# Kernel optimization log

Measured on AMD Instinct MI355X. Metric: run time of the kernel, lower is better.

## Reference

```python
import jax, jax.numpy as jnp
import numpy as np

DN = ('NCHW', 'OIHW', 'NCHW')

def conv2d(x, w, b, stride, pad):
    y = jax.lax.conv_general_dilated(x, w, (stride, stride), ((pad, pad), (pad, pad)), dimension_numbers=DN)
    return y + b[None, :, None, None]

def convt2d(x, w, b):
    # torch ConvTranspose2d(k=4, stride=2, padding=1); torch weight layout [Cin, Cout, kH, kW]
    wf = jnp.flip(w, (2, 3)).transpose(1, 0, 2, 3)  # -> [Cout, Cin, kH, kW]
    y = jax.lax.conv_general_dilated(x, wf, (1, 1), ((2, 2), (2, 2)), lhs_dilation=(2, 2), dimension_numbers=DN)
    return y + b[None, :, None, None]

def setup_inputs() -> dict:
    key = jax.random.key(0)
    ks = jax.random.split(key, 20)
    Hc, E, K = 128, 256, 8192
    s = lambda k, shape, fan: jax.random.normal(k, shape, jnp.float32) * (1.0 / np.sqrt(fan))
    inp = {
        'x': jax.random.normal(ks[0], (4, 3, 256, 256), jnp.float32),
        'enc_w1': s(ks[1], (Hc, 3, 4, 4), 3 * 16), 'enc_b1': jnp.zeros((Hc,), jnp.float32),
        'enc_w2': s(ks[2], (Hc, Hc, 4, 4), Hc * 16), 'enc_b2': jnp.zeros((Hc,), jnp.float32),
        'enc_w3': s(ks[3], (Hc, Hc, 3, 3), Hc * 9), 'enc_b3': jnp.zeros((Hc,), jnp.float32),
        'qconv_w': s(ks[4], (E, Hc, 1, 1), Hc), 'qconv_b': jnp.zeros((E,), jnp.float32),
        'codebook': jax.random.uniform(ks[5], (K, E), jnp.float32, -1.0 / K, 1.0 / K),
        'pqconv_w': s(ks[6], (Hc, E, 1, 1), E), 'pqconv_b': jnp.zeros((Hc,), jnp.float32),
        'dec_w1': s(ks[7], (Hc, Hc, 3, 3), Hc * 9), 'dec_b1': jnp.zeros((Hc,), jnp.float32),
        'dect_w2': s(ks[8], (Hc, Hc, 4, 4), Hc * 16), 'dect_b2': jnp.zeros((Hc,), jnp.float32),
        'dect_w3': s(ks[9], (Hc, 3, 4, 4), Hc * 16), 'dect_b3': jnp.zeros((3,), jnp.float32),
    }
    return inp

def quantize(z, codebook):
    B, C, H, W = z.shape
    zf = z.transpose(0, 2, 3, 1).reshape(-1, C)  # [N, C]
    d = (jnp.sum(zf * zf, axis=1, keepdims=True)
         + jnp.sum(codebook * codebook, axis=1)
         - 2.0 * zf @ codebook.T)  # [N, K]
    indices = jnp.argmin(d, axis=1)
    quant = codebook[indices].reshape(B, H, W, C).transpose(0, 3, 1, 2)
    commit_loss = jnp.mean((jax.lax.stop_gradient(quant) - z) ** 2)
    quant = z + jax.lax.stop_gradient(quant - z)  # straight-through
    return quant, indices, commit_loss

def reference(x, enc_w1, enc_b1, enc_w2, enc_b2, enc_w3, enc_b3, qconv_w, qconv_b,
              codebook, pqconv_w, pqconv_b, dec_w1, dec_b1, dect_w2, dect_b2, dect_w3, dect_b3):
    h = jax.nn.relu(conv2d(x, enc_w1, enc_b1, 2, 1))
    h = jax.nn.relu(conv2d(h, enc_w2, enc_b2, 2, 1))
    h = conv2d(h, enc_w3, enc_b3, 1, 1)
    h = conv2d(h, qconv_w, qconv_b, 1, 0)
    quant, indices, commit_loss = quantize(h, codebook)
    q = conv2d(quant, pqconv_w, pqconv_b, 1, 0)
    d = jax.nn.relu(conv2d(q, dec_w1, dec_b1, 1, 1))
    d = jax.nn.relu(convt2d(d, dect_w2, dect_b2))
    recon = convt2d(d, dect_w3, dect_b3)
    return recon, commit_loss, indices
```

## Files before the change

### kernel.cpp

```cpp
#include <hip/hip_runtime.h>

#define OFF_A     ((size_t)0)
#define OFF_BINFO ((size_t)8388608)
#define OFF_B     ((size_t)34611200)
#define OFF_C     ((size_t)43532288)
#define OFF_D     ((size_t)52453376)
#define OFF_E     ((size_t)69230592)
#define OFF_ZN    ((size_t)81813504)
#define OFF_CN    ((size_t)81879040)
#define OFF_IDX   ((size_t)81911808)
#define OFF_ACC   ((size_t)81977344)
#define OFF_WR2   ((size_t)81977600)
#define OFF_WR3   ((size_t)83026176)
#define OFF_QWT   ((size_t)83050752)
#define OFF_WD2   ((size_t)83181824)
#define OFF_WD3   ((size_t)85278976)
#define OFF_WD1   ((size_t)86458624)

#define VQ_MARGIN 1.2e-4f
#define LDSS 40

typedef __attribute__((ext_vector_type(8))) _Float16 f16x8;
typedef __attribute__((ext_vector_type(4))) float f32x4;

__device__ __forceinline__ unsigned fkey(float f) {
  unsigned u = __float_as_uint(f);
  return (u & 0x80000000u) ? ~u : (u | 0x80000000u);
}
__device__ __forceinline__ float funkey(unsigned k) {
  unsigned u = (k & 0x80000000u) ? (k ^ 0x80000000u) : ~k;
  return __uint_as_float(u);
}
__device__ __forceinline__ void padzero_img(float* base, int S, int t) {
  for (int e = t; e < 4 * S - 4; e += 256) {
    int rr, cc;
    if (e < S) { rr = 0; cc = e; }
    else if (e < 2 * S) { rr = S - 1; cc = e - S; }
    else { rr = ((e - 2 * S) >> 1) + 1; cc = (e & 1) ? (S - 1) : 0; }
    base[rr * S + cc] = 0.0f;
  }
}

__global__ __launch_bounds__(256) void prep_k(
    const float* __restrict__ dtw2, float* __restrict__ wr2,
    const float* __restrict__ dtw3, float* __restrict__ wr3,
    const float* __restrict__ qw,   float* __restrict__ qwT,
    const float* __restrict__ ew2,  double* __restrict__ wd2,
    const float* __restrict__ ew3,  double* __restrict__ wd3,
    const float* __restrict__ ew1,  double* __restrict__ wd1,
    float* __restrict__ xpad, float* __restrict__ h1p, float* __restrict__ h2p) {
  int b = blockIdx.x, t = threadIdx.x;
  if (b < 256) {
    int tid = b * 256 + t;
    int ci = tid & 127, co = (tid >> 7) & 127, cls = tid >> 14;
    int kh0 = 1 - (cls >> 1), kw0 = 1 - (cls & 1);
    const float* s = dtw2 + ((size_t)ci * 128 + co) * 16;
    float* d = wr2 + (size_t)tid * 4;
    d[0] = s[kh0 * 4 + kw0];       d[1] = s[kh0 * 4 + kw0 + 2];
    d[2] = s[(kh0 + 2) * 4 + kw0]; d[3] = s[(kh0 + 2) * 4 + kw0 + 2];
  } else if (b < 262) {
    int tid = (b - 256) * 256 + t;
    if (tid < 1536) {
      int ci = tid & 127, co = (tid >> 7) % 3, cls = tid / 384;
      int kh0 = 1 - (cls >> 1), kw0 = 1 - (cls & 1);
      const float* s = dtw3 + ((size_t)ci * 3 + co) * 16;
      float* d = wr3 + (size_t)tid * 4;
      d[0] = s[kh0 * 4 + kw0];       d[1] = s[kh0 * 4 + kw0 + 2];
      d[2] = s[(kh0 + 2) * 4 + kw0]; d[3] = s[(kh0 + 2) * 4 + kw0 + 2];
    }
  } else if (b < 390) {
    int tid = (b - 262) * 256 + t;
    int co = tid & 255, ci = tid >> 8;
    qwT[(size_t)ci * 256 + co] = qw[(size_t)co * 128 + ci];
  } else if (b < 1414) {
    int tid = (b - 390) * 256 + t;
    wd2[tid] = (double)ew2[tid];
  } else if (b < 1990) {
    int tid = (b - 1414) * 256 + t;
    wd3[tid] = (double)ew3[tid];
  } else if (b < 2014) {
    int tid = (b - 1990) * 256 + t;
    wd1[tid] = (double)ew1[tid];
  } else if (b < 2026) {
    padzero_img(xpad + (size_t)(b - 2014) * 66564, 258, t);
  } else if (b < 2538) {
    padzero_img(h1p + (size_t)(b - 2026) * 16900, 130, t);
  } else {
    padzero_img(h2p + (size_t)(b - 2538) * 4356, 66, t);
  }
}

__global__ __launch_bounds__(256) void padx_k(const float* __restrict__ x,
                                              float* __restrict__ xp) {
  int tid = blockIdx.x * 256 + threadIdx.x;
  int wo = tid & 255, ho = (tid >> 8) & 255, c = tid >> 16;
  xp[((size_t)c * 258 + ho + 1) * 258 + wo + 1] = x[tid];
}

__global__ __launch_bounds__(256) void conv1_k(
    const float* __restrict__ xp, const double* __restrict__ wd,
    const float* __restrict__ bias, float* __restrict__ h1p) {
  int b = blockIdx.x;
  int chunk = b & 63, cog = (b >> 6) & 15, n = b >> 10;
  int t = threadIdx.x;
  int wo = t & 127, ho = chunk * 2 + (t >> 7);
  int co0 = cog * 8;
  const float* xb = xp + (size_t)n * 3 * 66564 + (size_t)(2 * ho) * 258 + 2 * wo;
  double acc[8] = {};
  for (int ci = 0; ci < 3; ++ci) {
    const float* xc = xb + (size_t)ci * 66564;
    float cf[16];
#pragma unroll
    for (int kh = 0; kh < 4; ++kh)
#pragma unroll
      for (int kw = 0; kw < 4; ++kw) cf[kh * 4 + kw] = xc[kh * 258 + kw];
    const double* wp = wd + (size_t)co0 * 48 + ci * 16;
#pragma unroll
    for (int tp = 0; tp < 16; ++tp) {
      double xd = (double)cf[tp];
#pragma unroll
      for (int cc = 0; cc < 8; ++cc)
        acc[cc] = fma(xd, wp[(size_t)cc * 48 + tp], acc[cc]);
    }
  }
#pragma unroll
  for (int cc = 0; cc < 8; ++cc) {
    float r = (float)((double)bias[co0 + cc] + acc[cc]);
    h1p[(((size_t)n * 128 + co0 + cc) * 130 + ho + 1) * 130 + wo + 1] = fmaxf(r, 0.0f);
  }
}

__global__ __launch_bounds__(256) void conv2_k(
    const float* __restrict__ h1p, const double* __restrict__ wd,
    const float* __restrict__ bias, float* __restrict__ h2p) {
  int b = blockIdx.x;
  int chunk = b & 15, cog = (b >> 4) & 15, n = b >> 8;
  int t = threadIdx.x;
  int wo = t & 63, ho = chunk * 4 + (t >> 6);
  int co0 = cog * 8;
  const float* xb = h1p + (size_t)n * 128 * 16900 + (size_t)(2 * ho) * 130 + 2 * wo;
  double acc[8] = {};
  for (int ci = 0; ci < 128; ++ci) {
    const float* xc = xb + (size_t)ci * 16900;
    float cf[16];
#pragma unroll
    for (int kh = 0; kh < 4; ++kh)
#pragma unroll
      for (int kw = 0; kw < 4; ++kw) cf[kh * 4 + kw] = xc[kh * 130 + kw];
    const double* wp = wd + (size_t)co0 * 2048 + ci * 16;
#pragma unroll
    for (int tp = 0; tp < 16; ++tp) {
      double xd = (double)cf[tp];
#pragma unroll
      for (int cc = 0; cc < 8; ++cc)
        acc[cc] = fma(xd, wp[(size_t)cc * 2048 + tp], acc[cc]);
    }
  }
#pragma unroll
  for (int cc = 0; cc < 8; ++cc) {
    float r = (float)((double)bias[co0 + cc] + acc[cc]);
    h2p[(((size_t)n * 128 + co0 + cc) * 66 + ho + 1) * 66 + wo + 1] = fmaxf(r, 0.0f);
  }
}

__global__ __launch_bounds__(256) void conv3_k(
    const float* __restrict__ h2p, const double* __restrict__ wd,
    const float* __restrict__ bias, float* __restrict__ h3) {
  int b = blockIdx.x;
  int chunk = b & 15, cog = (b >> 4) & 15, n = b >> 8;
  int t = threadIdx.x;
  int wo = t & 63, ho = chunk * 4 + (t >> 6);
  int co0 = cog * 8;
  const float* xb = h2p + (size_t)n * 128 * 4356 + (size_t)ho * 66 + wo;
  double acc[8] = {};
  for (int ci = 0; ci < 128; ++ci) {
    const float* xc = xb + (size_t)ci * 4356;
    float cf[9];
#pragma unroll
    for (int kh = 0; kh < 3; ++kh)
#pragma unroll
      for (int kw = 0; kw < 3; ++kw) cf[kh * 3 + kw] = xc[kh * 66 + kw];
    const double* wp = wd + (size_t)co0 * 1152 + ci * 9;
#pragma unroll
    for (int tp = 0; tp < 9; ++tp) {
      double xd = (double)cf[tp];
#pragma unroll
      for (int cc = 0; cc < 8; ++cc)
        acc[cc] = fma(xd, wp[(size_t)cc * 1152 + tp], acc[cc]);
    }
  }
#pragma unroll
  for (int cc = 0; cc < 8; ++cc)
    h3[(((size_t)n * 128 + co0 + cc) << 12) + (ho << 6) + wo] =
        (float)((double)bias[co0 + cc] + acc[cc]);
}

__global__ __launch_bounds__(256) void qconv_z_k(
    const float* __restrict__ h3, const float* __restrict__ wT,
    const float* __restrict__ bias, float* __restrict__ zf,
    _Float16* __restrict__ Ap, float* __restrict__ znb) {
  __shared__ double wsum[4];
  int p  = blockIdx.x;
  int co = threadIdx.x;
  int n  = p >> 12;
  int hw = p & 4095;
  const float* xp = h3 + ((size_t)n * 128) * 4096 + hw;
  double a[4] = {0.0, 0.0, 0.0, 0.0};
  for (int ci = 0; ci < 128; ci += 4) {
#pragma unroll
    for (int u = 0; u < 4; ++u) {
      float xv = xp[(size_t)(ci + u) * 4096];
      a[u] = fma((double)xv, (double)wT[(size_t)(ci + u) * 256 + co], a[u]);
    }
  }
  double acc = (double)bias[co] + ((a[0] + a[1]) + (a[2] + a[3]));
  float zv = (float)acc;
  zf[(size_t)p * 256 + co] = zv;
  Ap[(size_t)p * 256 + co] = (_Float16)zv;
  float xx = zv * zv;
  double s = (double)xx;
#pragma unroll
  for (int off = 32; off > 0; off >>= 1) s += __shfl_down(s, off, 64);
  if ((co & 63) == 0) wsum[co >> 6] = s;
  __syncthreads();
  if (co == 0) znb[p] = (float)((wsum[0] + wsum[1]) + (wsum[2] + wsum[3]));
}

__global__ __launch_bounds__(256) void cbprep_k(
    const float* __restrict__ cb, _Float16* __restrict__ Bp,
    float* __restrict__ cnb) {
  __shared__ double wsum[4];
  int k = blockIdx.x, t = threadIdx.x;
  float c = cb[(size_t)k * 256 + t];
  Bp[(size_t)k * 256 + t] = (_Float16)(c * 512.0f);
  float xx = c * c;
  double s = (double)xx;
#pragma unroll
  for (int off = 32; off > 0; off >>= 1) s += __shfl_down(s, off, 64);
  if ((t & 63) == 0) wsum[t >> 6] = s;
  __syncthreads();
  if (t == 0) cnb[k] = (float)((wsum[0] + wsum[1]) + (wsum[2] + wsum[3]));
}

__global__ __launch_bounds__(256, 2) void vq_gemm_k(
    const _Float16* __restrict__ Ah, const _Float16* __restrict__ Bh,
    const float* __restrict__ cnArr, int4* __restrict__ binfo) {
  __shared__ __align__(16) _Float16 As[128 * LDSS];
  __shared__ __align__(16) _Float16 Bs[128 * LDSS];
  __shared__ unsigned loc[128];
  __shared__ int cnt_sh[128];
  __shared__ int cand_sh[128][2];
  const int t = threadIdx.x;
  const int w = t >> 6, L = t & 63;
  const int mb = blockIdx.x >> 6;
  const int nb = blockIdx.x & 63;
  const int m0 = mb << 7, n0 = nb << 7;
  if (t < 128) { loc[t] = 0xFFFFFFFFu; cnt_sh[t] = 0; }
  f32x4 acc[4][4] = {};
  const int wr = (w >> 1) << 6, wc = (w & 1) << 6;
  const int srow = L >> 2, kg = L & 3;
  const int q = L >> 4, ln = L & 15;
  for (int kk = 0; kk < 256; kk += 32) {
    __syncthreads();
#pragma unroll
    for (int c = 0; c < 2; ++c) {
      const int row = (w << 5) + (c << 4) + srow;
      const f16x8 av = *(const f16x8*)(Ah + (size_t)(m0 + row) * 256 + kk + kg * 8);
      *(f16x8*)(&As[row * LDSS + kg * 8]) = av;
      const f16x8 bv = *(const f16x8*)(Bh + (size_t)(n0 + row) * 256 + kk + kg * 8);
      *(f16x8*)(&Bs[row * LDSS + kg * 8]) = bv;
    }
    __syncthreads();
    f16x8 af[4], bf[4];
#pragma unroll
    for (int i = 0; i < 4; ++i)
      af[i] = *(const f16x8*)(&As[(wr + 16 * i + ln) * LDSS + q * 8]);
#pragma unroll
    for (int j = 0; j < 4; ++j)
      bf[j] = *(const f16x8*)(&Bs[(wc + 16 * j + ln) * LDSS + q * 8]);
#pragma unroll
    for (int i = 0; i < 4; ++i)
#pragma unroll
      for (int j = 0; j < 4; ++j)
        acc[i][j] = __builtin_amdgcn_mfma_f32_16x16x32_f16(af[i], bf[j], acc[i][j], 0, 0, 0);
  }
  float cnv[4];
#pragma unroll
  for (int j = 0; j < 4; ++j) cnv[j] = cnArr[n0 + wc + 16 * j + ln];
#pragma unroll
  for (int i = 0; i < 4; ++i)
#pragma unroll
    for (int r = 0; r < 4; ++r) {
      float mn = 3.4e38f;
#pragma unroll
      for (int j = 0; j < 4; ++j)
        mn = fminf(mn, fmaf(-0.00390625f, acc[i][j][r], cnv[j]));
      atomicMin(&loc[wr + 16 * i + 4 * q + r], fkey(mn));
    }
  __syncthreads();
#pragma unroll
  for (int i = 0; i < 4; ++i)
#pragma unroll
    for (int r = 0; r < 4; ++r) {
      const int rib = wr + 16 * i + 4 * q + r;
      const float thr = funkey(loc[rib]) + VQ_MARGIN;
#pragma unroll
      for (int j = 0; j < 4; ++j) {
        float s = fmaf(-0.00390625f, acc[i][j][r], cnv[j]);
        if (s <= thr) {
          int slot = atomicAdd(&cnt_sh[rib], 1);
          if (slot < 2) cand_sh[rib][slot] = n0 + wc + 16 * j + ln;
        }
      }
    }
  __syncthreads();
  if (t < 128) {
    int4 v;
    v.x = cnt_sh[t];
    v.y = cand_sh[t][0];
    v.z = cand_sh[t][1];
    v.w = (int)__float_as_uint(funkey(loc[t]));
    binfo[(size_t)(m0 + t) * 64 + nb] = v;
  }
}

__global__ __launch_bounds__(256) void vq_phase3_k(
    const float* __restrict__ zf, const float* __restrict__ cb,
    const float* __restrict__ znArr, const float* __restrict__ cnArr,
    const int4* __restrict__ binfo, int* __restrict__ idxOut,
    float* __restrict__ accum) {
  if (blockIdx.x == 0 && threadIdx.x == 0) *accum = 0.0f;
  const int lane = threadIdx.x & 63;
  const int r = blockIdx.x * 4 + (threadIdx.x >> 6);
  const float* zr = zf + (size_t)r * 256;
  double z4[4];
#pragma unroll
  for (int j = 0; j < 4; ++j) z4[j] = (double)zr[lane + (j << 6)];
  const float znr = znArr[r];
  int4 b = binfo[(size_t)r * 64 + lane];
  float bv = __uint_as_float((unsigned)b.w);
  float m = bv;
#pragma unroll
  for (int off = 32; off > 0; off >>= 1) m = fminf(m, __shfl_down(m, off, 64));
  m = __shfl(m, 0, 64);
  const float thr = m + VQ_MARGIN;
  unsigned long long mask = __ballot(bv <= thr);
  float bestd = 3.4e38f;
  int bestk = 0x7fffffff;
  while (mask) {
    const int nb = (int)__builtin_ctzll(mask);
    mask &= mask - 1;
    const int c  = __shfl(b.x, nb, 64);
    const int k0 = __shfl(b.y, nb, 64);
    const int k1 = __shfl(b.z, nb, 64);
    const int nsc = (c <= 2) ? c : 128;
    for (int s2 = 0; s2 < nsc; ++s2) {
      const int k = (c <= 2) ? (s2 == 0 ? k0 : k1) : (nb * 128 + s2);
      const float* ck = cb + (size_t)k * 256;
      double p = 0.0;
#pragma unroll
      for (int j = 0; j < 4; ++j)
        p = fma(z4[j], (double)ck[lane + (j << 6)], p);
#pragma unroll
      for (int off = 32; off > 0; off >>= 1) p += __shfl_down(p, off, 64);
      if (lane == 0) {
        float mm2 = (float)(2.0 * p);
        float t1 = znr + cnArr[k];
        float d = t1 - mm2;
        if (d < bestd || (d == bestd && k < bestk)) { bestd = d; bestk = k; }
      }
    }
  }
  if (lane == 0) idxOut[r] = bestk;
}

__global__ __launch_bounds__(256) void commit_k(
    const float* __restrict__ zf, const float* __restrict__ cb,
    const int* __restrict__ idxArr, float* __restrict__ accum,
    float* __restrict__ outIdxF) {
  __shared__ float wsum[4];
  const int p = blockIdx.x;
  const int t = threadIdx.x;
  const int k = idxArr[p];
  float d = cb[(size_t)k * 256 + t] - zf[(size_t)p * 256 + t];
  float v = d * d;
#pragma unroll
  for (int off = 32; off > 0; off >>= 1) v += __shfl_down(v, off, 64);
  if ((t & 63) == 0) wsum[t >> 6] = v;
  __syncthreads();
  if (t == 0) {
    atomicAdd(accum, wsum[0] + wsum[1] + wsum[2] + wsum[3]);
    outIdxF[p] = (float)k;
  }
}

__global__ __launch_bounds__(256) void pc_k(const float* __restrict__ cb,
                                            const float* __restrict__ pw,
                                            float* __restrict__ PC) {
  int tid = blockIdx.x * 256 + threadIdx.x;
  int co = tid & 127, k = tid >> 7;
  const float* c = cb + (size_t)k * 256;
  const float* w = pw + (size_t)co * 256;
  float a0 = 0.0f, a1 = 0.0f, a2 = 0.0f, a3 = 0.0f;
  for (int ci = 0; ci < 256; ci += 4) {
    a0 = fmaf(c[ci], w[ci], a0);
    a1 = fmaf(c[ci + 1], w[ci + 1], a1);
    a2 = fmaf(c[ci + 2], w[ci + 2], a2);
    a3 = fmaf(c[ci + 3], w[ci + 3], a3);
  }
  PC[tid] = (a0 + a1) + (a2 + a3);
}

__global__ __launch_bounds__(256) void padzero_dec_k(
    float* __restrict__ qbufp, float* __restrict__ d1p, float* __restrict__ d2p) {
  int b = blockIdx.x, t = threadIdx.x;
  if (b < 512)       padzero_img(qbufp + (size_t)b * 4356, 66, t);
  else if (b < 1024) padzero_img(d1p + (size_t)(b - 512) * 4356, 66, t);
  else               padzero_img(d2p + (size_t)(b - 1024) * 16900, 130, t);
}

__global__ __launch_bounds__(256) void gather_pc_k(
    const float* __restrict__ PC, const int* __restrict__ idxArr,
    const float* __restrict__ pb, float* __restrict__ qp) {
  int tid = blockIdx.x * 256 + threadIdx.x;
  int hw = tid & 4095;
  int co = (tid >> 12) & 127;
  int n  = tid >> 19;
  int p  = (n << 12) + hw;
  int h = hw >> 6, w2 = hw & 63;
  qp[(((size_t)n * 128 + co) * 66 + h + 1) * 66 + w2 + 1] =
      PC[(size_t)idxArr[p] * 128 + co] + pb[co];
}

__global__ __launch_bounds__(256) void dconv1_k(
    const float* __restrict__ qp, const float* __restrict__ w,
    const float* __restrict__ bias, float* __restrict__ d1p) {
  int b = blockIdx.x;
  int chunk = b & 15, cog = (b >> 4) & 15, n = b >> 8;
  int t = threadIdx.x;
  int wo = t & 63, ho = chunk * 4 + (t >> 6);
  int co0 = cog * 8;
  const float* xb = qp + (size_t)n * 128 * 4356 + (size_t)ho * 66 + wo;
  float acc[8] = {};
  for (int ci = 0; ci < 128; ++ci) {
    const float* xc = xb + (size_t)ci * 4356;
    float xv[9];
#pragma unroll
    for (int kh = 0; kh < 3; ++kh)
#pragma unroll
      for (int kw = 0; kw < 3; ++kw) xv[kh * 3 + kw] = xc[kh * 66 + kw];
#pragma unroll
    for (int cc = 0; cc < 8; ++cc) {
      const float* wp = w + (size_t)(co0 + cc) * 1152 + ci * 9;
#pragma unroll
      for (int tp = 0; tp < 9; ++tp)
        acc[cc] = fmaf(xv[tp], wp[tp], acc[cc]);
    }
  }
#pragma unroll
  for (int cc = 0; cc < 8; ++cc)
    d1p[(((size_t)n * 128 + co0 + cc) * 66 + ho + 1) * 66 + wo + 1] =
        fmaxf(bias[co0 + cc] + acc[cc], 0.0f);
}

__global__ __launch_bounds__(256) void convt2_k(
    const float* __restrict__ xp, const float* __restrict__ wr,
    const float* __restrict__ bias, float* __restrict__ y) {
  int b = blockIdx.x;
  int chunk = b & 15, cls = (b >> 4) & 3, cog = (b >> 6) & 15, n = b >> 10;
  int cph = cls >> 1, cpw = cls & 1;
  int t = threadIdx.x;
  int wb = t & 63, i = chunk * 4 + (t >> 6);
  int co0 = cog * 8;
  int ho = 2 * i + cph, wo = 2 * wb + cpw;
  int r0 = i + 1 + cph, r1 = r0 - 1;
  int c0 = wb + 1 + cpw, c1 = c0 - 1;
  const float* xb = xp + (size_t)n * 128 * 4356;
  float acc[8] = {};
  for (int ci = 0; ci < 128; ++ci) {
    const float* xc = xb + (size_t)ci * 4356;
    float x00 = xc[r0 * 66 + c0], x01 = xc[r0 * 66 + c1];
    float x10 = xc[r1 * 66 + c0], x11 = xc[r1 * 66 + c1];
#pragma unroll
    for (int cc = 0; cc < 8; ++cc) {
      const float* w4 = wr + (((size_t)cls * 128 + co0 + cc) * 128 + ci) * 4;
      acc[cc] = fmaf(x00, w4[0], acc[cc]);
      acc[cc] = fmaf(x01, w4[1], acc[cc]);
      acc[cc] = fmaf(x10, w4[2], acc[cc]);
      acc[cc] = fmaf(x11, w4[3], acc[cc]);
    }
  }
#pragma unroll
  for (int cc = 0; cc < 8; ++cc)
    y[(((size_t)n * 128 + co0 + cc) * 130 + ho + 1) * 130 + wo + 1] =
        fmaxf(bias[co0 + cc] + acc[cc], 0.0f);
}

__global__ __launch_bounds__(256) void convt3_k(
    const float* __restrict__ xp, const float* __restrict__ wr,
    const float* __restrict__ bias, float* __restrict__ y,
    const float* __restrict__ accum, float* __restrict__ outLoss) {
  int b = blockIdx.x;
  if (b == 0 && threadIdx.x == 0) *outLoss = *accum * (1.0f / 4194304.0f);
  int chunk = b & 63, cls = (b >> 6) & 3, n = b >> 8;
  int cph = cls >> 1, cpw = cls & 1;
  int t = threadIdx.x;
  int wb = t & 127, i = chunk * 2 + (t >> 7);
  int ho = 2 * i + cph, wo = 2 * wb + cpw;
  int r0 = i + 1 + cph, r1 = r0 - 1;
  int c0 = wb + 1 + cpw, c1 = c0 - 1;
  const float* xb = xp + (size_t)n * 128 * 16900;
  float acc[3] = {0.0f, 0.0f, 0.0f};
  for (int ci = 0; ci < 128; ++ci) {
    const float* xc = xb + (size_t)ci * 16900;
    float x00 = xc[r0 * 130 + c0], x01 = xc[r0 * 130 + c1];
    float x10 = xc[r1 * 130 + c0], x11 = xc[r1 * 130 + c1];
#pragma unroll
    for (int cc = 0; cc < 3; ++cc) {
      const float* w4 = wr + (((size_t)cls * 3 + cc) * 128 + ci) * 4;
      acc[cc] = fmaf(x00, w4[0], acc[cc]);
      acc[cc] = fmaf(x01, w4[1], acc[cc]);
      acc[cc] = fmaf(x10, w4[2], acc[cc]);
      acc[cc] = fmaf(x11, w4[3], acc[cc]);
    }
  }
#pragma unroll
  for (int cc = 0; cc < 3; ++cc)
    y[(((size_t)n * 3 + cc) << 16) + (ho << 8) + wo] = bias[cc] + acc[cc];
}

extern "C" void kernel_launch(void* const* d_in, const int* in_sizes, int n_in,
                              void* d_out, int out_size, void* d_ws, size_t ws_size,
                              hipStream_t stream) {
  const float* x    = (const float*)d_in[0];
  const float* ew1  = (const float*)d_in[1];
  const float* eb1  = (const float*)d_in[2];
  const float* ew2  = (const float*)d_in[3];
  const float* eb2  = (const float*)d_in[4];
  const float* ew3  = (const float*)d_in[5];
  const float* eb3  = (const float*)d_in[6];
  const float* qw   = (const float*)d_in[7];
  const float* qb   = (const float*)d_in[8];
  const float* cb   = (const float*)d_in[9];
  const float* pw   = (const float*)d_in[10];
  const float* pb   = (const float*)d_in[11];
  const float* dw1  = (const float*)d_in[12];
  const float* db1  = (const float*)d_in[13];
  const float* dtw2 = (const float*)d_in[14];
  const float* dtb2 = (const float*)d_in[15];
  const float* dtw3 = (const float*)d_in[16];
  const float* dtb3 = (const float*)d_in[17];

  char* wsb = (char*)d_ws;
  float*    h1p  = (float*)(wsb + OFF_A);
  _Float16* Ap   = (_Float16*)(wsb + OFF_A);
  int4*     binfo= (int4*)(wsb + OFF_BINFO);
  float*    d2p  = (float*)(wsb + OFF_A);
  float*    h2p  = (float*)(wsb + OFF_B);
  float*    qbufp= (float*)(wsb + OFF_B);
  float*    xpad = (float*)(wsb + OFF_C);
  float*    h3   = (float*)(wsb + OFF_C);
  float*    d1p  = (float*)(wsb + OFF_C);
  float*    zff  = (float*)(wsb + OFF_D);
  _Float16* Bp   = (_Float16*)(wsb + OFF_E);
  float*    PC   = (float*)(wsb + OFF_E);
  float*    znb  = (float*)(wsb + OFF_ZN);
  float*    cnb  = (float*)(wsb + OFF_CN);
  int*      idxb = (int*)(wsb + OFF_IDX);
  float*    accum= (float*)(wsb + OFF_ACC);
  float*    wr2  = (float*)(wsb + OFF_WR2);
  float*    wr3  = (float*)(wsb + OFF_WR3);
  float*    qwT  = (float*)(wsb + OFF_QWT);
  double*   wd2  = (double*)(wsb + OFF_WD2);
  double*   wd3  = (double*)(wsb + OFF_WD3);
  double*   wd1  = (double*)(wsb + OFF_WD1);

  float* out      = (float*)d_out;
  float* outLoss  = out + 786432;
  float* outIdxF  = out + 786433;

  hipLaunchKernelGGL(prep_k, dim3(3050), dim3(256), 0, stream,
                     dtw2, wr2, dtw3, wr3, qw, qwT, ew2, wd2, ew3, wd3,
                     ew1, wd1, xpad, h1p, h2p);

  hipLaunchKernelGGL(padx_k,    dim3(3072),  dim3(256), 0, stream, x, xpad);
  hipLaunchKernelGGL(conv1_k,   dim3(4096),  dim3(256), 0, stream, xpad, wd1, eb1, h1p);
  hipLaunchKernelGGL(conv2_k,   dim3(1024),  dim3(256), 0, stream, h1p, wd2, eb2, h2p);
  hipLaunchKernelGGL(conv3_k,   dim3(1024),  dim3(256), 0, stream, h2p, wd3, eb3, h3);
  hipLaunchKernelGGL(qconv_z_k, dim3(16384), dim3(256), 0, stream, h3, qwT, qb, zff, Ap, znb);

  hipLaunchKernelGGL(cbprep_k,    dim3(8192),  dim3(256), 0, stream, cb, Bp, cnb);
  hipLaunchKernelGGL(vq_gemm_k,   dim3(8192),  dim3(256), 0, stream, Ap, Bp, cnb, binfo);
  hipLaunchKernelGGL(vq_phase3_k, dim3(4096),  dim3(256), 0, stream, zff, cb, znb, cnb, binfo, idxb, accum);
  hipLaunchKernelGGL(commit_k,    dim3(16384), dim3(256), 0, stream, zff, cb, idxb, accum, outIdxF);

  hipLaunchKernelGGL(pc_k,          dim3(4096), dim3(256), 0, stream, cb, pw, PC);
  hipLaunchKernelGGL(padzero_dec_k, dim3(1536), dim3(256), 0, stream, qbufp, d1p, d2p);
  hipLaunchKernelGGL(gather_pc_k,   dim3(8192), dim3(256), 0, stream, PC, idxb, pb, qbufp);
  hipLaunchKernelGGL(dconv1_k,      dim3(1024), dim3(256), 0, stream, qbufp, dw1, db1, d1p);
  hipLaunchKernelGGL(convt2_k,      dim3(4096), dim3(256), 0, stream, d1p, wr2, dtb2, d2p);
  hipLaunchKernelGGL(convt3_k,      dim3(1024), dim3(256), 0, stream, d2p, wr3, dtb3, out, accum, outLoss);
}
```

Measured before the change: 1.442 ms.

## Split input-channel reduction across two halves in conv2/conv3 and pre-reduce VQ row minima

conv2_k and conv3_k now run 512 threads per block, with each half reducing over 64 input channels. The two partial double sums are combined through shared memory, which doubles parallelism and gives more waves to hide FP64 latency. A software double-buffered load of input patches is added to overlap loads with FMAs. In the VQ GEMM, row minima are reduced with wave shuffles before a single atomicMin per row, which cuts LDS atomic contention. The costs are extra shared memory, a barrier, and a changed summation order in double precision, which is negligible.

Measured after the change: 2.612 ms. 81.2% more time.

```diff
diff --git a/kernel.cpp b/kernel.cpp
--- a/kernel.cpp
+++ b/kernel.cpp
@@ -38,6 +38,44 @@
     else if (e < 2 * S) { rr = S - 1; cc = e - S; }
     else { rr = ((e - 2 * S) >> 1) + 1; cc = (e & 1) ? (S - 1) : 0; }
     base[rr * S + cc] = 0.0f;
+  }
+}
+
+__device__ __forceinline__ void c2_load(const float* xb, int ci, float* buf) {
+  const float* xc = xb + (size_t)ci * 16900;
+#pragma unroll
+  for (int kh = 0; kh < 4; ++kh)
+#pragma unroll
+    for (int kw = 0; kw < 4; ++kw) buf[kh * 4 + kw] = xc[kh * 130 + kw];
+}
+__device__ __forceinline__ void c2_fma(const double* wb, int ci, const float* buf,
+                                       double* acc) {
+  const double* wp = wb + (size_t)ci * 16;
+#pragma unroll
+  for (int tp = 0; tp < 16; ++tp) {
+    double xd = (double)buf[tp];
+#pragma unroll
+    for (int cc = 0; cc < 8; ++cc)
+      acc[cc] = fma(xd, wp[(size_t)cc * 2048 + tp], acc[cc]);
+  }
+}
+
+__device__ __forceinline__ void c3_load(const float* xb, int ci, float* buf) {
+  const float* xc = xb + (size_t)ci * 4356;
+#pragma unroll
+  for (int kh = 0; kh < 3; ++kh)
+#pragma unroll
+    for (int kw = 0; kw < 3; ++kw) buf[kh * 3 + kw] = xc[kh * 66 + kw];
+}
+__device__ __forceinline__ void c3_fma(const double* wb, int ci, const float* buf,
+                                       double* acc) {
+  const double* wp = wb + (size_t)ci * 9;
+#pragma unroll
+  for (int tp = 0; tp < 9; ++tp) {
+    double xd = (double)buf[tp];
+#pragma unroll
+    for (int cc = 0; cc < 8; ++cc)
+      acc[cc] = fma(xd, wp[(size_t)cc * 1152 + tp], acc[cc]);
   }
 }
 
@@ -130,69 +168,84 @@
   }
 }
 
-__global__ __launch_bounds__(256) void conv2_k(
+__global__ __launch_bounds__(512) void conv2_k(
     const float* __restrict__ h1p, const double* __restrict__ wd,
     const float* __restrict__ bias, float* __restrict__ h2p) {
+  __shared__ double accsh[256][8];
   int b = blockIdx.x;
   int chunk = b & 15, cog = (b >> 4) & 15, n = b >> 8;
   int t = threadIdx.x;
-  int wo = t & 63, ho = chunk * 4 + (t >> 6);
+  int tl = t & 255, half = t >> 8;
+  int wo = tl & 63, ho = chunk * 4 + (tl >> 6);
   int co0 = cog * 8;
   const float* xb = h1p + (size_t)n * 128 * 16900 + (size_t)(2 * ho) * 130 + 2 * wo;
+  const double* wb = wd + (size_t)co0 * 2048;
   double acc[8] = {};
-  for (int ci = 0; ci < 128; ++ci) {
-    const float* xc = xb + (size_t)ci * 16900;
-    float cf[16];
-#pragma unroll
-    for (int kh = 0; kh < 4; ++kh)
-#pragma unroll
-      for (int kw = 0; kw < 4; ++kw) cf[kh * 4 + kw] = xc[kh * 130 + kw];
-    const double* wp = wd + (size_t)co0 * 2048 + ci * 16;
-#pragma unroll
-    for (int tp = 0; tp < 16; ++tp) {
-      double xd = (double)cf[tp];
-#pragma unroll
-      for (int cc = 0; cc < 8; ++cc)
-        acc[cc] = fma(xd, wp[(size_t)cc * 2048 + tp], acc[cc]);
-    }
-  }
-#pragma unroll
-  for (int cc = 0; cc < 8; ++cc) {
-    float r = (float)((double)bias[co0 + cc] + acc[cc]);
-    h2p[(((size_t)n * 128 + co0 + cc) * 66 + ho + 1) * 66 + wo + 1] = fmaxf(r, 0.0f);
-  }
-}
-
-__global__ __launch_bounds__(256) void conv3_k(
+  const int ci0 = half << 6;
+  float cfA[16], cfB[16];
+  c2_load(xb, ci0, cfA);
+  for (int ci = ci0; ci < ci0 + 62; ci += 2) {
+    c2_load(xb, ci + 1, cfB);
+    c2_fma(wb, ci, cfA, acc);
+    c2_load(xb, ci + 2, cfA);
+    c2_fma(wb, ci + 1, cfB, acc);
+  }
+  c2_load(xb, ci0 + 63, cfB);
+  c2_fma(wb, ci0 + 62, cfA, acc);
+  c2_fma(wb, ci0 + 63, cfB, acc);
+  if (half) {
+#pragma unroll
+    for (int cc = 0; cc < 8; ++cc) accsh[tl][cc] = acc[cc];
+  }
+  __syncthreads();
+  if (!half) {
+#pragma unroll
+    for (int cc = 0; cc < 8; ++cc) {
+      double tot = acc[cc] + accsh[tl][cc];
+      float r = (float)((double)bias[co0 + cc] + tot);
+      h2p[(((size_t)n * 128 + co0 + cc) * 66 + ho + 1) * 66 + wo + 1] = fmaxf(r, 0.0f);
+    }
+  }
+}
+
+__global__ __launch_bounds__(512) void conv3_k(
     const float* __restrict__ h2p, const double* __restrict__ wd,
     const float* __restrict__ bias, float* __restrict__ h3) {
+  __shared__ double accsh[256][8];
   int b = blockIdx.x;
   int chunk = b & 15, cog = (b >> 4) & 15, n = b >> 8;
   int t = threadIdx.x;
-  int wo = t & 63, ho = chunk * 4 + (t >> 6);
+  int tl = t & 255, half = t >> 8;
+  int wo = tl & 63, ho = chunk * 4 + (tl >> 6);
   int co0 = cog * 8;
   const float* xb = h2p + (size_t)n * 128 * 4356 + (size_t)ho * 66 + wo;
+  const double* wb = wd + (size_t)co0 * 1152;
   double acc[8] = {};
-  for (int ci = 0; ci < 128; ++ci) {
-    const float* xc = xb + (size_t)ci * 4356;
-    float cf[9];
-#pragma unroll
-    for (int kh = 0; kh < 3; ++kh)
-#pragma unroll
-      for (int kw = 0; kw < 3; ++kw) cf[kh * 3 + kw] = xc[kh * 66 + kw];
-    const double* wp = wd + (size_t)co0 * 1152 + ci * 9;
-#pragma unroll
-    for (int tp = 0; tp < 9; ++tp) {
-      double xd = (double)cf[tp];
-#pragma unroll
-      for (int cc = 0; cc < 8; ++cc)
-        acc[cc] = fma(xd, wp[(size_t)cc * 1152 + tp], acc[cc]);
-    }
-  }
-#pragma unroll
-  for (int cc = 0; cc < 8; ++cc)
-    h3[(((size_t)n * 128 + co0 + cc) << 12) + (ho << 6) + wo] =
-        (float)((double)bias[co0 + cc] + acc[cc]);
+  const int ci0 = half << 6;
+  float cfA[9], cfB[9];
+  c3_load(xb, ci0, cfA);
+  for (int ci = ci0; ci < ci0 + 62; ci += 2) {
+    c3_load(xb, ci + 1, cfB);
+    c3_fma(wb, ci, cfA, acc);
+    c3_load(xb, ci + 2, cfA);
+    c3_fma(wb, ci + 1, cfB, acc);
+  }
+  c3_load(xb, ci0 + 63, cfB);
+  c3_fma(wb, ci0 + 62, cfA, acc);
+  c3_fma(wb, ci0 + 63, cfB, acc);
+  if (half) {
+#pragma unroll
+    for (int cc = 0; cc < 8; ++cc) accsh[tl][cc] = acc[cc];
+  }
+  __syncthreads();
+  if (!half) {
+#pragma unroll
+    for (int cc = 0; cc < 8; ++cc) {
+      double tot = acc[cc] + accsh[tl][cc];
+      h3[(((size_t)n * 128 + co0 + cc) << 12) + (ho << 6) + wo] =
+          (float)((double)bias[co0 + cc] + tot);
+    }
+  }
 }
 
 __global__ __launch_bounds__(256) void qconv_z_k(
@@ -295,7 +348,10 @@
 #pragma unroll
       for (int j = 0; j < 4; ++j)
         mn = fminf(mn, fmaf(-0.00390625f, acc[i][j][r], cnv[j]));
-      atomicMin(&loc[wr + 16 * i + 4 * q + r], fkey(mn));
+#pragma unroll
+      for (int s = 1; s < 16; s <<= 1)
+        mn = fminf(mn, __shfl_xor(mn, s, 64));
+      if (ln == 0) atomicMin(&loc[wr + 16 * i + 4 * q + r], fkey(mn));
     }
   __syncthreads();
 #pragma unroll
@@ -585,8 +641,8 @@
 
   hipLaunchKernelGGL(padx_k,    dim3(3072),  dim3(256), 0, stream, x, xpad);
   hipLaunchKernelGGL(conv1_k,   dim3(4096),  dim3(256), 0, stream, xpad, wd1, eb1, h1p);
-  hipLaunchKernelGGL(conv2_k,   dim3(1024),  dim3(256), 0, stream, h1p, wd2, eb2, h2p);
-  hipLaunchKernelGGL(conv3_k,   dim3(1024),  dim3(256), 0, stream, h2p, wd3, eb3, h3);
+  hipLaunchKernelGGL(conv2_k,   dim3(1024),  dim3(512), 0, stream, h1p, wd2, eb2, h2p);
+  hipLaunchKernelGGL(conv3_k,   dim3(1024),  dim3(512), 0, stream, h2p, wd3, eb3, h3);
   hipLaunchKernelGGL(qconv_z_k, dim3(16384), dim3(256), 0, stream, h3, qwT, qb, zff, Ap, znb);
 
   hipLaunchKernelGGL(cbprep_k,    dim3(8192),  dim3(256), 0, stream, cb, Bp, cnb);
```

## Stage conv input tiles in double-buffered LDS with register prefetch; wave-reduce VQ min

Applied to the files above, without the earlier changes.

Conv2, conv3 and dconv1 now copy each input-channel row tile into shared memory and prefetch the next channel into registers while computing the current one. The conv2 tile is de-interleaved into even and odd columns so stride-2 reads stay contiguous. The aim is to replace redundant, uncoalesced global gathers with LDS reads and to overlap load latency with FMA work. In the VQ kernel, the per-row minimum is reduced across 16 lanes with shuffles before a single atomicMin, which cuts LDS atomic traffic. The cost is an extra barrier per channel iteration and LDS pressure that may lower occupancy; the fp64 FMA work, likely the real bottleneck, is unchanged.

Result: slower. 2.041 ms (+41.6%).

```diff
diff --git a/kernel.cpp b/kernel.cpp
--- a/kernel.cpp
+++ b/kernel.cpp
@@ -38,6 +38,39 @@
     else if (e < 2 * S) { rr = S - 1; cc = e - S; }
     else { rr = ((e - 2 * S) >> 1) + 1; cc = (e & 1) ? (S - 1) : 0; }
     base[rr * S + cc] = 0.0f;
+  }
+}
+
+__device__ __forceinline__ void c2_fma(const double* wb, int ci, const float* buf,
+                                       double* acc) {
+  const double* wp = wb + (size_t)ci * 16;
+#pragma unroll
+  for (int tp = 0; tp < 16; ++tp) {
+    double xd = (double)buf[tp];
+#pragma unroll
+    for (int cc = 0; cc < 8; ++cc)
+      acc[cc] = fma(xd, wp[(size_t)cc * 2048 + tp], acc[cc]);
+  }
+}
+__device__ __forceinline__ void c3_fma(const double* wb, int ci, const float* buf,
+                                       double* acc) {
+  const double* wp = wb + (size_t)ci * 9;
+#pragma unroll
+  for (int tp = 0; tp < 9; ++tp) {
+    double xd = (double)buf[tp];
+#pragma unroll
+    for (int cc = 0; cc < 8; ++cc)
+      acc[cc] = fma(xd, wp[(size_t)cc * 1152 + tp], acc[cc]);
+  }
+}
+__device__ __forceinline__ void d1_fma(const float* w, int co0, int ci,
+                                       const float* buf, float* acc) {
+#pragma unroll
+  for (int cc = 0; cc < 8; ++cc) {
+    const float* wp = w + (size_t)(co0 + cc) * 1152 + ci * 9;
+#pragma unroll
+    for (int tp = 0; tp < 9; ++tp)
+      acc[cc] = fmaf(buf[tp], wp[tp], acc[cc]);
   }
 }
 
@@ -133,29 +166,59 @@
 __global__ __launch_bounds__(256) void conv2_k(
     const float* __restrict__ h1p, const double* __restrict__ wd,
     const float* __restrict__ bias, float* __restrict__ h2p) {
+  __shared__ float tile[2][1300];
   int b = blockIdx.x;
   int chunk = b & 15, cog = (b >> 4) & 15, n = b >> 8;
   int t = threadIdx.x;
-  int wo = t & 63, ho = chunk * 4 + (t >> 6);
+  int wo = t & 63, hor = t >> 6;
   int co0 = cog * 8;
-  const float* xb = h1p + (size_t)n * 128 * 16900 + (size_t)(2 * ho) * 130 + 2 * wo;
+  const float* gsrc = h1p + (size_t)n * 128 * 16900 + (size_t)(8 * chunk) * 130;
+  const double* wb = wd + (size_t)co0 * 2048;
   double acc[8] = {};
+#pragma unroll
+  for (int u = 0; u < 6; ++u) {
+    int e = t + (u << 8);
+    if (u < 5 || e < 1300) {
+      int r = e / 130, c = e - r * 130;
+      tile[0][r * 130 + ((c & 1) ? 65 : 0) + (c >> 1)] = gsrc[e];
+    }
+  }
+  __syncthreads();
   for (int ci = 0; ci < 128; ++ci) {
-    const float* xc = xb + (size_t)ci * 16900;
+    const int cur = ci & 1;
+    float stg[6];
+    if (ci < 127) {
+      const float* gs = gsrc + (size_t)(ci + 1) * 16900;
+#pragma unroll
+      for (int u = 0; u < 6; ++u) {
+        int e = t + (u << 8);
+        if (u < 5 || e < 1300) stg[u] = gs[e];
+      }
+    }
+    const float* tl = tile[cur];
     float cf[16];
 #pragma unroll
-    for (int kh = 0; kh < 4; ++kh)
-#pragma unroll
-      for (int kw = 0; kw < 4; ++kw) cf[kh * 4 + kw] = xc[kh * 130 + kw];
-    const double* wp = wd + (size_t)co0 * 2048 + ci * 16;
-#pragma unroll
-    for (int tp = 0; tp < 16; ++tp) {
-      double xd = (double)cf[tp];
-#pragma unroll
-      for (int cc = 0; cc < 8; ++cc)
-        acc[cc] = fma(xd, wp[(size_t)cc * 2048 + tp], acc[cc]);
-    }
-  }
+    for (int kh = 0; kh < 4; ++kh) {
+      const float* rowp = tl + (2 * hor + kh) * 130;
+#pragma unroll
+      for (int kw = 0; kw < 4; ++kw)
+        cf[kh * 4 + kw] = rowp[((kw & 1) ? 65 : 0) + wo + (kw >> 1)];
+    }
+    c2_fma(wb, ci, cf, acc);
+    if (ci < 127) {
+      float* td = tile[cur ^ 1];
+#pragma unroll
+      for (int u = 0; u < 6; ++u) {
+        int e = t + (u << 8);
+        if (u < 5 || e < 1300) {
+          int r = e / 130, c = e - r * 130;
+          td[r * 130 + ((c & 1) ? 65 : 0) + (c >> 1)] = stg[u];
+        }
+      }
+    }
+    __syncthreads();
+  }
+  int ho = chunk * 4 + hor;
 #pragma unroll
   for (int cc = 0; cc < 8; ++cc) {
     float r = (float)((double)bias[co0 + cc] + acc[cc]);
@@ -166,29 +229,51 @@
 __global__ __launch_bounds__(256) void conv3_k(
     const float* __restrict__ h2p, const double* __restrict__ wd,
     const float* __restrict__ bias, float* __restrict__ h3) {
+  __shared__ float tile[2][396];
   int b = blockIdx.x;
   int chunk = b & 15, cog = (b >> 4) & 15, n = b >> 8;
   int t = threadIdx.x;
-  int wo = t & 63, ho = chunk * 4 + (t >> 6);
+  int wo = t & 63, hor = t >> 6;
   int co0 = cog * 8;
-  const float* xb = h2p + (size_t)n * 128 * 4356 + (size_t)ho * 66 + wo;
+  const float* gsrc = h2p + (size_t)n * 128 * 4356 + (size_t)(4 * chunk) * 66;
+  const double* wb = wd + (size_t)co0 * 1152;
   double acc[8] = {};
+#pragma unroll
+  for (int u = 0; u < 2; ++u) {
+    int e = t + (u << 8);
+    if (u < 1 || e < 396) tile[0][e] = gsrc[e];
+  }
+  __syncthreads();
   for (int ci = 0; ci < 128; ++ci) {
-    const float* xc = xb + (size_t)ci * 4356;
+    const int cur = ci & 1;
+    float stg[2];
+    if (ci < 127) {
+      const float* gs = gsrc + (size_t)(ci + 1) * 4356;
+#pragma unroll
+      for (int u = 0; u < 2; ++u) {
+        int e = t + (u << 8);
+        if (u < 1 || e < 396) stg[u] = gs[e];
+      }
+    }
+    const float* tl = tile[cur];
     float cf[9];
 #pragma unroll
     for (int kh = 0; kh < 3; ++kh)
 #pragma unroll
-      for (int kw = 0; kw < 3; ++kw) cf[kh * 3 + kw] = xc[kh * 66 + kw];
-    const double* wp = wd + (size_t)co0 * 1152 + ci * 9;
-#pragma unroll
-    for (int tp = 0; tp < 9; ++tp) {
-      double xd = (double)cf[tp];
-#pragma unroll
-      for (int cc = 0; cc < 8; ++cc)
-        acc[cc] = fma(xd, wp[(size_t)cc * 1152 + tp], acc[cc]);
-    }
-  }
+      for (int kw = 0; kw < 3; ++kw)
+        cf[kh * 3 + kw] = tl[(hor + kh) * 66 + wo + kw];
+    c3_fma(wb, ci, cf, acc);
+    if (ci < 127) {
+      float* td = tile[cur ^ 1];
+#pragma unroll
+      for (int u = 0; u < 2; ++u) {
+        int e = t + (u << 8);
+        if (u < 1 || e < 396) td[e] = stg[u];
+      }
+    }
+    __syncthreads();
+  }
+  int ho = chunk * 4 + hor;
 #pragma unroll
   for (int cc = 0; cc < 8; ++cc)
     h3[(((size_t)n * 128 + co0 + cc) << 12) + (ho << 6) + wo] =
@@ -295,7 +380,10 @@
 #pragma unroll
       for (int j = 0; j < 4; ++j)
         mn = fminf(mn, fmaf(-0.00390625f, acc[i][j][r], cnv[j]));
-      atomicMin(&loc[wr + 16 * i + 4 * q + r], fkey(mn));
+#pragma unroll
+      for (int s = 1; s < 16; s <<= 1)
+        mn = fminf(mn, __shfl_xor(mn, s, 64));
+      if (ln == 0) atomicMin(&loc[wr + 16 * i + 4 * q + r], fkey(mn));
     }
   __syncthreads();
 #pragma unroll
@@ -435,28 +523,50 @@
 __global__ __launch_bounds__(256) void dconv1_k(
     const float* __restrict__ qp, const float* __restrict__ w,
     const float* __restrict__ bias, float* __restrict__ d1p) {
+  __shared__ float tile[2][396];
   int b = blockIdx.x;
   int chunk = b & 15, cog = (b >> 4) & 15, n = b >> 8;
   int t = threadIdx.x;
-  int wo = t & 63, ho = chunk * 4 + (t >> 6);
+  int wo = t & 63, hor = t >> 6;
   int co0 = cog * 8;
-  const float* xb = qp + (size_t)n * 128 * 4356 + (size_t)ho * 66 + wo;
+  const float* gsrc = qp + (size_t)n * 128 * 4356 + (size_t)(4 * chunk) * 66;
   float acc[8] = {};
+#pragma unroll
+  for (int u = 0; u < 2; ++u) {
+    int e = t + (u << 8);
+    if (u < 1 || e < 396) tile[0][e] = gsrc[e];
+  }
+  __syncthreads();
   for (int ci = 0; ci < 128; ++ci) {
-    const float* xc = xb + (size_t)ci * 4356;
-    float xv[9];
+    const int cur = ci & 1;
+    float stg[2];
+    if (ci < 127) {
+      const float* gs = gsrc + (size_t)(ci + 1) * 4356;
+#pragma unroll
+      for (int u = 0; u < 2; ++u) {
+        int e = t + (u << 8);
+        if (u < 1 || e < 396) stg[u] = gs[e];
+      }
+    }
+    const float* tl = tile[cur];
+    float cf[9];
 #pragma unroll
     for (int kh = 0; kh < 3; ++kh)
 #pragma unroll
-      for (int kw = 0; kw < 3; ++kw) xv[kh * 3 + kw] = xc[kh * 66 + kw];
-#pragma unroll
-    for (int cc = 0; cc < 8; ++cc) {
-      const float* wp = w + (size_t)(co0 + cc) * 1152 + ci * 9;
-#pragma unroll
-      for (int tp = 0; tp < 9; ++tp)
-        acc[cc] = fmaf(xv[tp], wp[tp], acc[cc]);
-    }
-  }
+      for (int kw = 0; kw < 3; ++kw)
+        cf[kh * 3 + kw] = tl[(hor + kh) * 66 + wo + kw];
+    d1_fma(w, co0, ci, cf, acc);
+    if (ci < 127) {
+      float* td = tile[cur ^ 1];
+#pragma unroll
+      for (int u = 0; u < 2; ++u) {
+        int e = t + (u << 8);
+        if (u < 1 || e < 396) td[e] = stg[u];
+      }
+    }
+    __syncthreads();
+  }
+  int ho = chunk * 4 + hor;
 #pragma unroll
   for (int cc = 0; cc < 8; ++cc)
     d1p[(((size_t)n * 128 + co0 + cc) * 66 + ho + 1) * 66 + wo + 1] =
```

## Run transposed conv2 on fp16 MFMA, vectorize conv2 loads, shuffle-reduce VQ min

Applied to the files above, without the earlier changes.

Rewrites the first transposed-conv decoder layer to use 16x16x32 fp16 MFMA instructions. The dconv1 output is now stored in fp16 and the transposed-conv weights are repacked to fp16 in the prep kernel, which replaces the scalar fp32 FMA loop. The encoder conv2 input loads become float2 vector loads. The VQ row-min now uses a wave shuffle reduction before a single LDS atomicMin instead of one atomic per lane. The fp16 activations and weights reduce precision in the decoder path.

Measured after the change: 1.387 ms. -3.8%, faster.

```diff
diff --git a/kernel.cpp b/kernel.cpp
--- a/kernel.cpp
+++ b/kernel.cpp
@@ -40,9 +40,18 @@
     base[rr * S + cc] = 0.0f;
   }
 }
+__device__ __forceinline__ void padzero_img_h(_Float16* base, int S, int t) {
+  for (int e = t; e < 4 * S - 4; e += 256) {
+    int rr, cc;
+    if (e < S) { rr = 0; cc = e; }
+    else if (e < 2 * S) { rr = S - 1; cc = e - S; }
+    else { rr = ((e - 2 * S) >> 1) + 1; cc = (e & 1) ? (S - 1) : 0; }
+    base[rr * S + cc] = (_Float16)0.0f;
+  }
+}
 
 __global__ __launch_bounds__(256) void prep_k(
-    const float* __restrict__ dtw2, float* __restrict__ wr2,
+    const float* __restrict__ dtw2, _Float16* __restrict__ wh2,
     const float* __restrict__ dtw3, float* __restrict__ wr3,
     const float* __restrict__ qw,   float* __restrict__ qwT,
     const float* __restrict__ ew2,  double* __restrict__ wd2,
@@ -55,9 +64,11 @@
     int ci = tid & 127, co = (tid >> 7) & 127, cls = tid >> 14;
     int kh0 = 1 - (cls >> 1), kw0 = 1 - (cls & 1);
     const float* s = dtw2 + ((size_t)ci * 128 + co) * 16;
-    float* d = wr2 + (size_t)tid * 4;
-    d[0] = s[kh0 * 4 + kw0];       d[1] = s[kh0 * 4 + kw0 + 2];
-    d[2] = s[(kh0 + 2) * 4 + kw0]; d[3] = s[(kh0 + 2) * 4 + kw0 + 2];
+    _Float16* d = wh2 + (size_t)tid * 4;
+    float d0 = s[kh0 * 4 + kw0];       float d1v = s[kh0 * 4 + kw0 + 2];
+    float d2v = s[(kh0 + 2) * 4 + kw0]; float d3v = s[(kh0 + 2) * 4 + kw0 + 2];
+    d[0] = (_Float16)d1v; d[1] = (_Float16)d0;
+    d[2] = (_Float16)d3v; d[3] = (_Float16)d2v;
   } else if (b < 262) {
     int tid = (b - 256) * 256 + t;
     if (tid < 1536) {
@@ -144,9 +155,12 @@
     const float* xc = xb + (size_t)ci * 16900;
     float cf[16];
 #pragma unroll
-    for (int kh = 0; kh < 4; ++kh)
-#pragma unroll
-      for (int kw = 0; kw < 4; ++kw) cf[kh * 4 + kw] = xc[kh * 130 + kw];
+    for (int kh = 0; kh < 4; ++kh) {
+      float2 p0 = *(const float2*)(xc + kh * 130);
+      float2 p1 = *(const float2*)(xc + kh * 130 + 2);
+      cf[kh * 4 + 0] = p0.x; cf[kh * 4 + 1] = p0.y;
+      cf[kh * 4 + 2] = p1.x; cf[kh * 4 + 3] = p1.y;
+    }
     const double* wp = wd + (size_t)co0 * 2048 + ci * 16;
 #pragma unroll
     for (int tp = 0; tp < 16; ++tp) {
@@ -295,7 +309,10 @@
 #pragma unroll
       for (int j = 0; j < 4; ++j)
         mn = fminf(mn, fmaf(-0.00390625f, acc[i][j][r], cnv[j]));
-      atomicMin(&loc[wr + 16 * i + 4 * q + r], fkey(mn));
+#pragma unroll
+      for (int s = 1; s < 16; s <<= 1)
+        mn = fminf(mn, __shfl_xor(mn, s, 64));
+      if (ln == 0) atomicMin(&loc[wr + 16 * i + 4 * q + r], fkey(mn));
     }
   __syncthreads();
 #pragma unroll
@@ -412,10 +429,11 @@
 }
 
 __global__ __launch_bounds__(256) void padzero_dec_k(
-    float* __restrict__ qbufp, float* __restrict__ d1p, float* __restrict__ d2p) {
+    float* __restrict__ qbufp, _Float16* __restrict__ d1pH,
+    float* __restrict__ d2p) {
   int b = blockIdx.x, t = threadIdx.x;
   if (b < 512)       padzero_img(qbufp + (size_t)b * 4356, 66, t);
-  else if (b < 1024) padzero_img(d1p + (size_t)(b - 512) * 4356, 66, t);
+  else if (b < 1024) padzero_img_h(d1pH + (size_t)(b - 512) * 4356, 66, t);
   else               padzero_img(d2p + (size_t)(b - 1024) * 16900, 130, t);
 }
 
@@ -434,7 +452,7 @@
 
 __global__ __launch_bounds__(256) void dconv1_k(
     const float* __restrict__ qp, const float* __restrict__ w,
-    const float* __restrict__ bias, float* __restrict__ d1p) {
+    const float* __restrict__ bias, _Float16* __restrict__ d1pH) {
   int b = blockIdx.x;
   int chunk = b & 15, cog = (b >> 4) & 15, n = b >> 8;
   int t = threadIdx.x;
@@ -459,41 +477,50 @@
   }
 #pragma unroll
   for (int cc = 0; cc < 8; ++cc)
-    d1p[(((size_t)n * 128 + co0 + cc) * 66 + ho + 1) * 66 + wo + 1] =
-        fmaxf(bias[co0 + cc] + acc[cc], 0.0f);
+    d1pH[(((size_t)n * 128 + co0 + cc) * 66 + ho + 1) * 66 + wo + 1] =
+        (_Float16)fmaxf(bias[co0 + cc] + acc[cc], 0.0f);
 }
 
 __global__ __launch_bounds__(256) void convt2_k(
-    const float* __restrict__ xp, const float* __restrict__ wr,
+    const _Float16* __restrict__ xh, const _Float16* __restrict__ wh,
     const float* __restrict__ bias, float* __restrict__ y) {
   int b = blockIdx.x;
-  int chunk = b & 15, cls = (b >> 4) & 3, cog = (b >> 6) & 15, n = b >> 10;
+  int i = b & 63, cog = (b >> 6) & 7, cls = (b >> 9) & 3, n = b >> 11;
   int cph = cls >> 1, cpw = cls & 1;
   int t = threadIdx.x;
-  int wb = t & 63, i = chunk * 4 + (t >> 6);
-  int co0 = cog * 8;
+  int wv = t >> 6, l = t & 63;
+  int q = l >> 4, ln = l & 15;
+  int wb = (wv << 4) + ln;
+  int co0 = cog << 4;
+  int r0 = i + 1 + cph, r1 = r0 - 1;
+  int c1 = wb + cpw;
+  int o0 = r0 * 66 + c1, o1 = r1 * 66 + c1;
+  const unsigned short* xb =
+      (const unsigned short*)xh + (size_t)n * 128 * 4356 + (size_t)(q * 2) * 4356;
+  const _Float16* ap = wh + (size_t)(cls * 128 + co0 + ln) * 512 + q * 8;
+  f32x4 acc = {0.0f, 0.0f, 0.0f, 0.0f};
+  for (int s = 0; s < 16; ++s) {
+    const unsigned short* pa = xb + (size_t)(s * 8) * 4356;
+    const unsigned short* pb2 = pa + 4356;
+    unsigned v0 = pa[o0], v1 = pa[o0 + 1];
+    unsigned v2 = pa[o1], v3 = pa[o1 + 1];
+    unsigned v4 = pb2[o0], v5 = pb2[o0 + 1];
+    unsigned v6 = pb2[o1], v7 = pb2[o1 + 1];
+    union { unsigned u[4]; f16x8 h; } bb;
+    bb.u[0] = v0 | (v1 << 16);
+    bb.u[1] = v2 | (v3 << 16);
+    bb.u[2] = v4 | (v5 << 16);
+    bb.u[3] = v6 | (v7 << 16);
+    const f16x8 af = *(const f16x8*)(ap + s * 32);
+    acc = __builtin_amdgcn_mfma_f32_16x16x32_f16(af, bb.h, acc, 0, 0, 0);
+  }
   int ho = 2 * i + cph, wo = 2 * wb + cpw;
-  int r0 = i + 1 + cph, r1 = r0 - 1;
-  int c0 = wb + 1 + cpw, c1 = c0 - 1;
-  const float* xb = xp + (size_t)n * 128 * 4356;
-  float acc[8] = {};
-  for (int ci = 0; ci < 128; ++ci) {
-    const float* xc = xb + (size_t)ci * 4356;
-    float x00 = xc[r0 * 66 + c0], x01 = xc[r0 * 66 + c1];
-    float x10 = xc[r1 * 66 + c0], x11 = xc[r1 * 66 + c1];
-#pragma unroll
-    for (int cc = 0; cc < 8; ++cc) {
-      const float* w4 = wr + (((size_t)cls * 128 + co0 + cc) * 128 + ci) * 4;
-      acc[cc] = fmaf(x00, w4[0], acc[cc]);
-      acc[cc] = fmaf(x01, w4[1], acc[cc]);
-      acc[cc] = fmaf(x10, w4[2], acc[cc]);
-      acc[cc] = fmaf(x11, w4[3], acc[cc]);
-    }
-  }
-#pragma unroll
-  for (int cc = 0; cc < 8; ++cc)
-    y[(((size_t)n * 128 + co0 + cc) * 130 + ho + 1) * 130 + wo + 1] =
-        fmaxf(bias[co0 + cc] + acc[cc], 0.0f);
+#pragma unroll
+  for (int r = 0; r < 4; ++r) {
+    int co = co0 + q * 4 + r;
+    y[(((size_t)n * 128 + co) * 130 + ho + 1) * 130 + wo + 1] =
+        fmaxf(bias[co] + acc[r], 0.0f);
+  }
 }
 
 __global__ __launch_bounds__(256) void convt3_k(
@@ -560,7 +587,7 @@
   float*    qbufp= (float*)(wsb + OFF_B);
   float*    xpad = (float*)(wsb + OFF_C);
   float*    h3   = (float*)(wsb + OFF_C);
-  float*    d1p  = (float*)(wsb + OFF_C);
+  _Float16* d1pH = (_Float16*)(wsb + OFF_C);
   float*    zff  = (float*)(wsb + OFF_D);
   _Float16* Bp   = (_Float16*)(wsb + OFF_E);
   float*    PC   = (float*)(wsb + OFF_E);
@@ -568,7 +595,7 @@
   float*    cnb  = (float*)(wsb + OFF_CN);
   int*      idxb = (int*)(wsb + OFF_IDX);
   float*    accum= (float*)(wsb + OFF_ACC);
-  float*    wr2  = (float*)(wsb + OFF_WR2);
+  _Float16* wh2  = (_Float16*)(wsb + OFF_WR2);
   float*    wr3  = (float*)(wsb + OFF_WR3);
   float*    qwT  = (float*)(wsb + OFF_QWT);
   double*   wd2  = (double*)(wsb + OFF_WD2);
@@ -580,7 +607,7 @@
   float* outIdxF  = out + 786433;
 
   hipLaunchKernelGGL(prep_k, dim3(3050), dim3(256), 0, stream,
-                     dtw2, wr2, dtw3, wr3, qw, qwT, ew2, wd2, ew3, wd3,
+                     dtw2, wh2, dtw3, wr3, qw, qwT, ew2, wd2, ew3, wd3,
                      ew1, wd1, xpad, h1p, h2p);
 
   hipLaunchKernelGGL(padx_k,    dim3(3072),  dim3(256), 0, stream, x, xpad);
@@ -595,9 +622,9 @@
   hipLaunchKernelGGL(commit_k,    dim3(16384), dim3(256), 0, stream, zff, cb, idxb, accum, outIdxF);
 
   hipLaunchKernelGGL(pc_k,          dim3(4096), dim3(256), 0, stream, cb, pw, PC);
-  hipLaunchKernelGGL(padzero_dec_k, dim3(1536), dim3(256), 0, stream, qbufp, d1p, d2p);
+  hipLaunchKernelGGL(padzero_dec_k, dim3(1536), dim3(256), 0, stream, qbufp, d1pH, d2p);
   hipLaunchKernelGGL(gather_pc_k,   dim3(8192), dim3(256), 0, stream, PC, idxb, pb, qbufp);
-  hipLaunchKernelGGL(dconv1_k,      dim3(1024), dim3(256), 0, stream, qbufp, dw1, db1, d1p);
-  hipLaunchKernelGGL(convt2_k,      dim3(4096), dim3(256), 0, stream, d1p, wr2, dtb2, d2p);
+  hipLaunchKernelGGL(dconv1_k,      dim3(1024), dim3(256), 0, stream, qbufp, dw1, db1, d1pH);
+  hipLaunchKernelGGL(convt2_k,      dim3(8192), dim3(256), 0, stream, d1pH, wh2, dtb2, d2p);
   hipLaunchKernelGGL(convt3_k,      dim3(1024), dim3(256), 0, stream, d2p, wr3, dtb3, out, accum, outLoss);
 }
```
